# Performance work log

Measured on AMD Instinct MI355X. Metric: run time of the kernel, lower is better.

The kernel has to match this reference:

```python
import jax, jax.numpy as jnp
import numpy as np

N_NODES = 131072
N_EDGES = 4194304
H1, H2 = 16, 1


def setup_inputs() -> dict:
    key = jax.random.key(0)
    k = jax.random.split(key, 6)
    x = jax.random.uniform(k[0], (N_NODES, 2), dtype=jnp.float32)
    edge_index = jax.random.randint(k[1], (2, N_EDGES), 0, N_NODES, dtype=jnp.int64)
    # GCNConv weights (glorot-ish scale) and zero biases
    W1 = jax.random.normal(k[2], (2, H1), dtype=jnp.float32) * 0.5
    b1 = jnp.zeros((H1,), dtype=jnp.float32)
    W2 = jax.random.normal(k[3], (H1, H2), dtype=jnp.float32) * 0.25
    b2 = jnp.zeros((H2,), dtype=jnp.float32)
    return {"x": x, "W1": W1, "b1": b1, "W2": W2, "b2": b2, "edge_index": edge_index}


def gcn_layer(x, W, b, src, dst, n):
    # PyG GCNConv: h = D^{-1/2} (A+I) D^{-1/2} (x W) + b  (self-loops already in src/dst)
    h = x @ W                                              # [N, F_out]
    deg = jax.ops.segment_sum(jnp.ones(dst.shape[0], h.dtype), dst, num_segments=n)
    dinv = jax.lax.rsqrt(deg)                              # deg >= 1 thanks to self-loops
    norm = dinv[src] * dinv[dst]                           # [E+N]
    out = jax.ops.segment_sum(h[src] * norm[:, None], dst, num_segments=n)
    return out + b


def reference(x, W1, b1, W2, b2, edge_index):
    n = x.shape[0]
    loops = jnp.arange(n, dtype=edge_index.dtype)
    src = jnp.concatenate([edge_index[0], loops])          # add self-loops once
    dst = jnp.concatenate([edge_index[1], loops])
    h = jax.nn.relu(gcn_layer(x, W1, b1, src, dst, n))
    h = gcn_layer(h, W2, b2, src, dst, n)                  # [N, 1]
    scores = jax.nn.sigmoid(h)
    return scores[edge_index[0]]                           # gather per-edge source score [E, 1]
```

## Files before the change

### kernel.cpp

```cpp
#include <hip/hip_runtime.h>
#include <cmath>

typedef unsigned int uint;
typedef unsigned short u16;

constexpr int N  = 131072;
constexpr int E  = 4194304;
constexpr int F  = 16;
constexpr int NB = 512;
constexpr int NBLK  = 512;
constexpr int SCT   = 512;
constexpr int CHUNK = 8192;
constexpr int EPT   = 16;
constexpr int CAPB  = 9216;
constexpr int LPN   = 16;

__global__ void __launch_bounds__(SCT) k_scatter(
        const int* __restrict__ src, const int* __restrict__ dst,
        uint* __restrict__ part, u16* __restrict__ cnt16, u16* __restrict__ dir16) {
    __shared__ uint h[NB];
    __shared__ uint wsum[8];
    __shared__ uint vals[CHUNK];
    int t = threadIdx.x, g = blockIdx.x;
    int lane = t & 63, w = t >> 6;
    h[t] = 0;
    __syncthreads();
    int d[EPT], s[EPT];
    const int4* src4 = (const int4*)src;
    const int4* dst4 = (const int4*)dst;
    int base4 = g * (CHUNK / 4);
#pragma unroll
    for (int k = 0; k < EPT / 4; ++k) {
        int4 d4 = dst4[base4 + k * SCT + t];
        int4 s4 = src4[base4 + k * SCT + t];
        d[4 * k + 0] = d4.x; d[4 * k + 1] = d4.y; d[4 * k + 2] = d4.z; d[4 * k + 3] = d4.w;
        s[4 * k + 0] = s4.x; s[4 * k + 1] = s4.y; s[4 * k + 2] = s4.z; s[4 * k + 3] = s4.w;
        atomicAdd(&h[d4.x >> 8], 1u);
        atomicAdd(&h[d4.y >> 8], 1u);
        atomicAdd(&h[d4.z >> 8], 1u);
        atomicAdd(&h[d4.w >> 8], 1u);
    }
    __syncthreads();
    uint v = h[t];
    uint sv = v;
#pragma unroll
    for (int off = 1; off < 64; off <<= 1) {
        uint n = __shfl_up(sv, off);
        if (lane >= off) sv += n;
    }
    if (lane == 63) wsum[w] = sv;
    __syncthreads();
    uint wo = 0;
    for (int i = 0; i < w; ++i) wo += wsum[i];
    sv += wo;
    uint ex = sv - v;
    cnt16[(size_t)t * NBLK + g] = (u16)v;
    dir16[(size_t)t * NBLK + g] = (u16)ex;
    __syncthreads();
    h[t] = ex;
    __syncthreads();
#pragma unroll
    for (int k = 0; k < EPT; ++k) {
        int b = d[k] >> 8;
        uint slot = atomicAdd(&h[b], 1u);
        vals[slot] = ((uint)s[k] << 8) | (uint)(d[k] & 255);
    }
    __syncthreads();
    uint4* part4 = (uint4*)(part + (size_t)g * CHUNK);
    const uint4* vals4 = (const uint4*)vals;
#pragma unroll
    for (int k = 0; k < EPT / 4; ++k)
        part4[k * SCT + t] = vals4[k * SCT + t];
}

__global__ void __launch_bounds__(SCT) k_sort(
        const uint* __restrict__ part, const u16* __restrict__ cnt16,
        const u16* __restrict__ dir16, const float* __restrict__ x,
        uint* __restrict__ part2, uint* __restrict__ csr, uint* __restrict__ cend,
        float* __restrict__ dinv, float2* __restrict__ y) {
    __shared__ uint hw[8 * 256];
    __shared__ uint cnt[256];
    __shared__ uint sc[256];
    __shared__ uint wsum[4];
    __shared__ uint srt[CAPB];
    int t = threadIdx.x, b = blockIdx.x;
    int lane = t & 63, w = t >> 6;
#pragma unroll
    for (int k = 0; k < 4; ++k) hw[k * SCT + t] = 0;
    __syncthreads();
    uint segc = cnt16[(size_t)b * NBLK + t];
    const uint* seg = part + (size_t)t * CHUNK + dir16[(size_t)b * NBLK + t];
    for (uint j = 0; j < segc; ++j)
        atomicAdd(&hw[w * 256 + (seg[j] & 255u)], 1u);
    __syncthreads();
    if (t < 256) {
        uint tot = 0;
#pragma unroll
        for (int k = 0; k < 8; ++k) {
            uint c = hw[k * 256 + t];
            hw[k * 256 + t] = tot;
            tot += c;
        }
        cnt[t] = tot;
        uint sv = tot;
#pragma unroll
        for (int off = 1; off < 64; off <<= 1) {
            uint n = __shfl_up(sv, off);
            if (lane >= off) sv += n;
        }
        if (lane == 63) wsum[t >> 6] = sv;
        sc[t] = sv;
    }
    __syncthreads();
    if (t < 256) {
        uint wo = 0;
        for (int i = 0; i < (t >> 6); ++i) wo += wsum[i];
        sc[t] += wo;
    }
    __syncthreads();
    for (uint j = 0; j < segc; ++j) {
        uint pk = seg[j];
        uint bin = pk & 255u;
        uint slot = (sc[bin] - cnt[bin]) + atomicAdd(&hw[w * 256 + bin], 1u);
        if (slot < (uint)CAPB) srt[slot] = pk >> 8;
    }
    __syncthreads();
    uint L = sc[255];
    if (L > (uint)CAPB) L = CAPB;
    uint* out2 = part2 + (size_t)b * CAPB;
    for (uint i = t; i < L; i += SCT) out2[i] = srt[i];
    if (t < 256) {
        int node = (b << 8) + t;
        uint o0 = sc[t] - cnt[t];
        csr[node]  = (uint)b * CAPB + o0;
        cend[node] = (uint)b * CAPB + sc[t];
        float di = rsqrtf(1.0f + (float)cnt[t]);
        dinv[node] = di;
        float2 xv = ((const float2*)x)[node];
        y[node] = make_float2(di * xv.x, di * xv.y);
    }
}

__global__ void k_l1(const uint* __restrict__ srcs, const uint* __restrict__ csr,
                     const uint* __restrict__ cend,
                     const float2* __restrict__ y, const float* __restrict__ dinv,
                     const float* __restrict__ W1, const float* __restrict__ b1,
                     const float* __restrict__ W2, float* __restrict__ g2) {
    int tid = blockIdx.x * blockDim.x + threadIdx.x;
    int node = tid >> 4, lane = tid & (LPN - 1);
    uint o0 = csr[node];
    uint o1 = cend[node];
    float A0 = 0.0f, A1 = 0.0f;
    for (uint j = o0 + lane; j < o1; j += LPN) {
        float2 ys = y[srcs[j]];
        A0 += ys.x; A1 += ys.y;
    }
    A0 += __shfl_xor(A0, 1); A0 += __shfl_xor(A0, 2);
    A0 += __shfl_xor(A0, 4); A0 += __shfl_xor(A0, 8);
    A1 += __shfl_xor(A1, 1); A1 += __shfl_xor(A1, 2);
    A1 += __shfl_xor(A1, 4); A1 += __shfl_xor(A1, 8);
    float di = dinv[node];
    float2 yn = y[node];
    A0 = di * (A0 + yn.x);
    A1 = di * (A1 + yn.y);
    int f = lane;
    float v = fmaf(A0, W1[f], fmaf(A1, W1[F + f], b1[f]));
    float acc = fmaxf(v, 0.0f) * W2[f];
    acc += __shfl_xor(acc, 1); acc += __shfl_xor(acc, 2);
    acc += __shfl_xor(acc, 4); acc += __shfl_xor(acc, 8);
    if (lane == 0) g2[node] = di * acc;
}

__global__ void k_l2(const uint* __restrict__ srcs, const uint* __restrict__ csr,
                     const uint* __restrict__ cend,
                     const float* __restrict__ g2, const float* __restrict__ dinv,
                     const float* __restrict__ b2, float* __restrict__ scores) {
    int tid = blockIdx.x * blockDim.x + threadIdx.x;
    int node = tid >> 4, lane = tid & (LPN - 1);
    uint o0 = csr[node];
    uint o1 = cend[node];
    float acc = 0.0f;
    for (uint j = o0 + lane; j < o1; j += LPN) acc += g2[srcs[j]];
    acc += __shfl_xor(acc, 1); acc += __shfl_xor(acc, 2);
    acc += __shfl_xor(acc, 4); acc += __shfl_xor(acc, 8);
    if (lane == 0) {
        float v = fmaf(dinv[node], acc + g2[node], b2[0]);
        scores[node] = 1.0f / (1.0f + expf(-v));
    }
}

__global__ void k_out(const int* __restrict__ src, const float* __restrict__ scores,
                      float* __restrict__ out) {
    int i = blockIdx.x * blockDim.x + threadIdx.x;
    if (i >= E / 4) return;
    int4 s4 = ((const int4*)src)[i];
    float4 o;
    o.x = scores[s4.x];
    o.y = scores[s4.y];
    o.z = scores[s4.z];
    o.w = scores[s4.w];
    ((float4*)out)[i] = o;
}

extern "C" void kernel_launch(void* const* d_in, const int* in_sizes, int n_in,
                              void* d_out, int out_size, void* d_ws, size_t ws_size,
                              hipStream_t stream) {
    const float* x  = (const float*)d_in[0];
    const float* W1 = (const float*)d_in[1];
    const float* b1 = (const float*)d_in[2];
    const float* W2 = (const float*)d_in[3];
    const float* b2 = (const float*)d_in[4];
    const int*   ei = (const int*)d_in[5];
    const int* src = ei;
    const int* dst = ei + E;

    u16* cnt16   = (u16*)d_ws;
    u16* dir16   = cnt16 + (size_t)NB * NBLK;
    uint* csr    = (uint*)(dir16 + (size_t)NB * NBLK);
    uint* cend   = csr + N;
    float* dinv  = (float*)(cend + N);
    float2* y    = (float2*)(dinv + N);
    float* g2    = (float*)(y + N);
    float* scores = g2 + N;
    uint* part2  = (uint*)(scores + N);

    uint* part  = (uint*)d_out;
    float* out  = (float*)d_out;

    k_scatter<<<NBLK,            SCT, 0, stream>>>(src, dst, part, cnt16, dir16);
    k_sort   <<<NB,              SCT, 0, stream>>>(part, cnt16, dir16, x, part2,
                                                   csr, cend, dinv, y);
    k_l1     <<<(N * LPN) / 256, 256, 0, stream>>>(part2, csr, cend, y, dinv,
                                                   W1, b1, W2, g2);
    k_l2     <<<(N * LPN) / 256, 256, 0, stream>>>(part2, csr, cend, g2, dinv,
                                                   b2, scores);
    k_out    <<<E / 4 / 256,     256, 0, stream>>>(src, scores, out);
}
```

Baseline: 205.7 us.

## Replace per-bucket CSR sort with unsorted bucket lists and LDS atomic aggregation

The second pass no longer sorts each 256-node bucket into CSR order. Instead it gathers the bucket's packed (src,dst-low) entries with a binary search over segment prefix sums, so reads are coalesced, and stores them unsorted together with a bucket length. Both GCN layers now run one block per bucket and accumulate neighbour contributions through per-wave shared-memory float atomics, then reduce across waves and apply the dense transform per node. This removes the per-segment serial loops and second counting pass of the sort, plus the csr/cend arrays. The cost is LDS float atomic contention, and the summation order is no longer deterministic.

```diff
diff --git a/kernel.cpp b/kernel.cpp
--- a/kernel.cpp
+++ b/kernel.cpp
@@ -13,7 +13,6 @@
 constexpr int CHUNK = 8192;
 constexpr int EPT   = 16;
 constexpr int CAPB  = 9216;
-constexpr int LPN   = 16;
 
 __global__ void __launch_bounds__(SCT) k_scatter(
         const int* __restrict__ src, const int* __restrict__ dst,
@@ -73,117 +72,124 @@
         part4[k * SCT + t] = vals4[k * SCT + t];
 }
 
-__global__ void __launch_bounds__(SCT) k_sort(
+__global__ void __launch_bounds__(SCT) k_gather(
         const uint* __restrict__ part, const u16* __restrict__ cnt16,
         const u16* __restrict__ dir16, const float* __restrict__ x,
-        uint* __restrict__ part2, uint* __restrict__ csr, uint* __restrict__ cend,
+        uint* __restrict__ part2, uint* __restrict__ blen,
         float* __restrict__ dinv, float2* __restrict__ y) {
+    __shared__ uint ps[NB + 1];
+    __shared__ uint segoff[NB];
     __shared__ uint hw[8 * 256];
-    __shared__ uint cnt[256];
-    __shared__ uint sc[256];
-    __shared__ uint wsum[4];
-    __shared__ uint srt[CAPB];
+    __shared__ uint wsum[8];
+    __shared__ uint stage[CAPB];
     int t = threadIdx.x, b = blockIdx.x;
     int lane = t & 63, w = t >> 6;
 #pragma unroll
     for (int k = 0; k < 4; ++k) hw[k * SCT + t] = 0;
-    __syncthreads();
-    uint segc = cnt16[(size_t)b * NBLK + t];
-    const uint* seg = part + (size_t)t * CHUNK + dir16[(size_t)b * NBLK + t];
-    for (uint j = 0; j < segc; ++j)
-        atomicAdd(&hw[w * 256 + (seg[j] & 255u)], 1u);
-    __syncthreads();
+    uint len = cnt16[(size_t)b * NBLK + t];
+    segoff[t] = (uint)t * CHUNK + dir16[(size_t)b * NBLK + t];
+    uint sv = len;
+#pragma unroll
+    for (int off = 1; off < 64; off <<= 1) {
+        uint n = __shfl_up(sv, off);
+        if (lane >= off) sv += n;
+    }
+    if (lane == 63) wsum[w] = sv;
+    __syncthreads();
+    uint wo = 0;
+    for (int i = 0; i < w; ++i) wo += wsum[i];
+    ps[t] = sv + wo - len;
+    uint L = 0;
+#pragma unroll
+    for (int i = 0; i < 8; ++i) L += wsum[i];
+    if (t == 0) ps[NB] = L;
+    __syncthreads();
+    for (uint i = t; i < L; i += SCT) {
+        uint lo = 0, hi = NB;
+        while (hi - lo > 1) {
+            uint mid = (lo + hi) >> 1;
+            if (ps[mid] <= i) lo = mid; else hi = mid;
+        }
+        uint pk = part[segoff[lo] + (i - ps[lo])];
+        if (i < (uint)CAPB) stage[i] = pk;
+        atomicAdd(&hw[w * 256 + (pk & 255u)], 1u);
+    }
+    __syncthreads();
+    uint Lc = (L > (uint)CAPB) ? (uint)CAPB : L;
+    uint* o2 = part2 + (size_t)b * CAPB;
+    for (uint i = t; i < Lc; i += SCT) o2[i] = stage[i];
+    if (t == 0) blen[b] = Lc;
     if (t < 256) {
-        uint tot = 0;
-#pragma unroll
-        for (int k = 0; k < 8; ++k) {
-            uint c = hw[k * 256 + t];
-            hw[k * 256 + t] = tot;
-            tot += c;
-        }
-        cnt[t] = tot;
-        uint sv = tot;
-#pragma unroll
-        for (int off = 1; off < 64; off <<= 1) {
-            uint n = __shfl_up(sv, off);
-            if (lane >= off) sv += n;
-        }
-        if (lane == 63) wsum[t >> 6] = sv;
-        sc[t] = sv;
-    }
-    __syncthreads();
-    if (t < 256) {
-        uint wo = 0;
-        for (int i = 0; i < (t >> 6); ++i) wo += wsum[i];
-        sc[t] += wo;
-    }
-    __syncthreads();
-    for (uint j = 0; j < segc; ++j) {
-        uint pk = seg[j];
-        uint bin = pk & 255u;
-        uint slot = (sc[bin] - cnt[bin]) + atomicAdd(&hw[w * 256 + bin], 1u);
-        if (slot < (uint)CAPB) srt[slot] = pk >> 8;
-    }
-    __syncthreads();
-    uint L = sc[255];
-    if (L > (uint)CAPB) L = CAPB;
-    uint* out2 = part2 + (size_t)b * CAPB;
-    for (uint i = t; i < L; i += SCT) out2[i] = srt[i];
-    if (t < 256) {
+        uint c = 0;
+#pragma unroll
+        for (int k = 0; k < 8; ++k) c += hw[k * 256 + t];
         int node = (b << 8) + t;
-        uint o0 = sc[t] - cnt[t];
-        csr[node]  = (uint)b * CAPB + o0;
-        cend[node] = (uint)b * CAPB + sc[t];
-        float di = rsqrtf(1.0f + (float)cnt[t]);
+        float di = rsqrtf(1.0f + (float)c);
         dinv[node] = di;
         float2 xv = ((const float2*)x)[node];
         y[node] = make_float2(di * xv.x, di * xv.y);
     }
 }
 
-__global__ void k_l1(const uint* __restrict__ srcs, const uint* __restrict__ csr,
-                     const uint* __restrict__ cend,
-                     const float2* __restrict__ y, const float* __restrict__ dinv,
-                     const float* __restrict__ W1, const float* __restrict__ b1,
-                     const float* __restrict__ W2, float* __restrict__ g2) {
-    int tid = blockIdx.x * blockDim.x + threadIdx.x;
-    int node = tid >> 4, lane = tid & (LPN - 1);
-    uint o0 = csr[node];
-    uint o1 = cend[node];
-    float A0 = 0.0f, A1 = 0.0f;
-    for (uint j = o0 + lane; j < o1; j += LPN) {
-        float2 ys = y[srcs[j]];
-        A0 += ys.x; A1 += ys.y;
-    }
-    A0 += __shfl_xor(A0, 1); A0 += __shfl_xor(A0, 2);
-    A0 += __shfl_xor(A0, 4); A0 += __shfl_xor(A0, 8);
-    A1 += __shfl_xor(A1, 1); A1 += __shfl_xor(A1, 2);
-    A1 += __shfl_xor(A1, 4); A1 += __shfl_xor(A1, 8);
-    float di = dinv[node];
-    float2 yn = y[node];
-    A0 = di * (A0 + yn.x);
-    A1 = di * (A1 + yn.y);
-    int f = lane;
-    float v = fmaf(A0, W1[f], fmaf(A1, W1[F + f], b1[f]));
-    float acc = fmaxf(v, 0.0f) * W2[f];
-    acc += __shfl_xor(acc, 1); acc += __shfl_xor(acc, 2);
-    acc += __shfl_xor(acc, 4); acc += __shfl_xor(acc, 8);
-    if (lane == 0) g2[node] = di * acc;
-}
-
-__global__ void k_l2(const uint* __restrict__ srcs, const uint* __restrict__ csr,
-                     const uint* __restrict__ cend,
-                     const float* __restrict__ g2, const float* __restrict__ dinv,
-                     const float* __restrict__ b2, float* __restrict__ scores) {
-    int tid = blockIdx.x * blockDim.x + threadIdx.x;
-    int node = tid >> 4, lane = tid & (LPN - 1);
-    uint o0 = csr[node];
-    uint o1 = cend[node];
-    float acc = 0.0f;
-    for (uint j = o0 + lane; j < o1; j += LPN) acc += g2[srcs[j]];
-    acc += __shfl_xor(acc, 1); acc += __shfl_xor(acc, 2);
-    acc += __shfl_xor(acc, 4); acc += __shfl_xor(acc, 8);
-    if (lane == 0) {
+__global__ void __launch_bounds__(SCT) k_l1(
+        const uint* __restrict__ part2, const uint* __restrict__ blen,
+        const float2* __restrict__ y, const float* __restrict__ dinv,
+        const float* __restrict__ W1, const float* __restrict__ b1,
+        const float* __restrict__ W2, float* __restrict__ g2) {
+    __shared__ float a0[8 * 256], a1[8 * 256];
+    int t = threadIdx.x, b = blockIdx.x, w = t >> 6;
+#pragma unroll
+    for (int k = 0; k < 4; ++k) { a0[k * SCT + t] = 0.0f; a1[k * SCT + t] = 0.0f; }
+    __syncthreads();
+    uint L = blen[b];
+    const uint* p = part2 + (size_t)b * CAPB;
+    for (uint i = t; i < L; i += SCT) {
+        uint pk = p[i];
+        float2 ys = y[pk >> 8];
+        atomicAdd(&a0[w * 256 + (pk & 255u)], ys.x);
+        atomicAdd(&a1[w * 256 + (pk & 255u)], ys.y);
+    }
+    __syncthreads();
+    if (t < 256) {
+        float A0 = 0.0f, A1 = 0.0f;
+#pragma unroll
+        for (int k = 0; k < 8; ++k) { A0 += a0[k * 256 + t]; A1 += a1[k * 256 + t]; }
+        int node = (b << 8) + t;
+        float di = dinv[node];
+        float2 yn = y[node];
+        A0 = di * (A0 + yn.x);
+        A1 = di * (A1 + yn.y);
+        float acc = 0.0f;
+#pragma unroll
+        for (int f = 0; f < F; ++f) {
+            float v = fmaf(A0, W1[f], fmaf(A1, W1[F + f], b1[f]));
+            acc = fmaf(fmaxf(v, 0.0f), W2[f], acc);
+        }
+        g2[node] = di * acc;
+    }
+}
+
+__global__ void __launch_bounds__(SCT) k_l2(
+        const uint* __restrict__ part2, const uint* __restrict__ blen,
+        const float* __restrict__ g2, const float* __restrict__ dinv,
+        const float* __restrict__ b2, float* __restrict__ scores) {
+    __shared__ float a[8 * 256];
+    int t = threadIdx.x, b = blockIdx.x, w = t >> 6;
+#pragma unroll
+    for (int k = 0; k < 4; ++k) a[k * SCT + t] = 0.0f;
+    __syncthreads();
+    uint L = blen[b];
+    const uint* p = part2 + (size_t)b * CAPB;
+    for (uint i = t; i < L; i += SCT) {
+        uint pk = p[i];
+        atomicAdd(&a[w * 256 + (pk & 255u)], g2[pk >> 8]);
+    }
+    __syncthreads();
+    if (t < 256) {
+        float acc = 0.0f;
+#pragma unroll
+        for (int k = 0; k < 8; ++k) acc += a[k * 256 + t];
+        int node = (b << 8) + t;
         float v = fmaf(dinv[node], acc + g2[node], b2[0]);
         scores[node] = 1.0f / (1.0f + expf(-v));
     }
@@ -214,25 +220,22 @@
     const int* src = ei;
     const int* dst = ei + E;
 
-    u16* cnt16   = (u16*)d_ws;
-    u16* dir16   = cnt16 + (size_t)NB * NBLK;
-    uint* csr    = (uint*)(dir16 + (size_t)NB * NBLK);
-    uint* cend   = csr + N;
-    float* dinv  = (float*)(cend + N);
-    float2* y    = (float2*)(dinv + N);
-    float* g2    = (float*)(y + N);
+    u16* cnt16    = (u16*)d_ws;
+    u16* dir16    = cnt16 + (size_t)NB * NBLK;
+    uint* blen    = (uint*)(dir16 + (size_t)NB * NBLK);
+    float* dinv   = (float*)(blen + NB);
+    float2* y     = (float2*)(dinv + N);
+    float* g2     = (float*)(y + N);
     float* scores = g2 + N;
-    uint* part2  = (uint*)(scores + N);
+    uint* part2   = (uint*)(scores + N);
 
     uint* part  = (uint*)d_out;
     float* out  = (float*)d_out;
 
-    k_scatter<<<NBLK,            SCT, 0, stream>>>(src, dst, part, cnt16, dir16);
-    k_sort   <<<NB,              SCT, 0, stream>>>(part, cnt16, dir16, x, part2,
-                                                   csr, cend, dinv, y);
-    k_l1     <<<(N * LPN) / 256, 256, 0, stream>>>(part2, csr, cend, y, dinv,
-                                                   W1, b1, W2, g2);
-    k_l2     <<<(N * LPN) / 256, 256, 0, stream>>>(part2, csr, cend, g2, dinv,
-                                                   b2, scores);
-    k_out    <<<E / 4 / 256,     256, 0, stream>>>(src, scores, out);
-}
+    k_scatter<<<NBLK,        SCT, 0, stream>>>(src, dst, part, cnt16, dir16);
+    k_gather <<<NB,          SCT, 0, stream>>>(part, cnt16, dir16, x, part2,
+                                               blen, dinv, y);
+    k_l1     <<<NB,          SCT, 0, stream>>>(part2, blen, y, dinv, W1, b1, W2, g2);
+    k_l2     <<<NB,          SCT, 0, stream>>>(part2, blen, g2, dinv, b2, scores);
+    k_out    <<<E / 4 / 256, 256, 0, stream>>>(src, scores, out);
+}
```

New measurement: 205.9 us. About the same (+0.1%).
